# Optimization experiments

Hardware: AMD Instinct MI355X
Metric: run time of the kernel (lower is better)

## Reference

```python
import jax, jax.numpy as jnp
import numpy as np

NQ = 8          # qubits -> 2^8 = 256 amplitudes
B = 32768       # batch

# ---- gate matrices (torchquantum conventions) ----

def _rx(t):
    c = jnp.cos(t / 2).astype(jnp.complex64)
    s = jnp.sin(t / 2).astype(jnp.complex64)
    return jnp.stack([jnp.stack([c, -1j * s]), jnp.stack([-1j * s, c])])

def _ry(t):
    c = jnp.cos(t / 2).astype(jnp.complex64)
    s = jnp.sin(t / 2).astype(jnp.complex64)
    return jnp.stack([jnp.stack([c, -s]), jnp.stack([s, c])])

def _rz(t):
    tc = t.astype(jnp.complex64)
    z = jnp.zeros((), jnp.complex64)
    return jnp.stack([jnp.stack([jnp.exp(-0.5j * tc), z]),
                      jnp.stack([z, jnp.exp(0.5j * tc)])])

def _u3(p):
    th, ph, lm = p[0], p[1], p[2]
    ct = jnp.cos(th / 2).astype(jnp.complex64)
    st = jnp.sin(th / 2).astype(jnp.complex64)
    eip = jnp.exp(1j * ph.astype(jnp.complex64))
    eil = jnp.exp(1j * lm.astype(jnp.complex64))
    return jnp.stack([jnp.stack([ct, -eil * st]),
                      jnp.stack([eip * st, eip * eil * ct])])

# ---- statevector ops; state shape [B] + [2]*NQ ----

def apply_1q(state, U, w):
    s = jnp.moveaxis(state, 1 + w, -1)
    s = jnp.einsum('ij,b...j->b...i', U, s)
    return jnp.moveaxis(s, -1, 1 + w)

def apply_ctrl(state, U, c, t):
    s = jnp.moveaxis(state, (1 + c, 1 + t), (-2, -1))
    s1 = jnp.einsum('ij,b...j->b...i', U, s[..., 1, :])
    s = jnp.concatenate([s[..., :1, :], s1[..., None, :]], axis=-2)
    return jnp.moveaxis(s, (-2, -1), (1 + c, 1 + t))

def expval_z(state, w):
    p = state.real ** 2 + state.imag ** 2
    axes = tuple(i for i in range(1, NQ + 1) if i != 1 + w)
    pm = jnp.sum(p, axis=axes)  # [B, 2]
    return pm[:, 0] - pm[:, 1]

def encode(x):
    # RY angle encoding: product state, amplitude per qubit = (cos(x/2), sin(x/2))
    a = jnp.stack([jnp.cos(x / 2), jnp.sin(x / 2)], -1).astype(jnp.complex64)  # [B,8,2]
    state = a[:, 0]
    for q in range(1, NQ):
        state = jnp.einsum('b...i,bj->b...ij', state, a[:, q])
    return state  # [B,2,2,...,2]

CR_PAIRS_1 = [(0, 1), (2, 3), (4, 5), (6, 7), (1, 2), (3, 4), (5, 6)]
CR_PAIRS_2 = [(1, 3), (5, 7), (3, 5)]

def branch(state, cr_fn, crp, u3p):
    # crp: [10] angles, u3p: [6,3]
    for i, (c, t) in enumerate(CR_PAIRS_1):
        state = apply_ctrl(state, cr_fn(crp[i]), c, t)
    # intermediate tqm.expval calls do not mutate the state -> omitted
    for i, w in enumerate([1, 3, 5, 7]):
        state = apply_1q(state, _u3(u3p[i]), w)
    for i, (c, t) in enumerate(CR_PAIRS_2):
        state = apply_ctrl(state, cr_fn(crp[7 + i]), c, t)
    state = apply_1q(state, _u3(u3p[4]), 3)
    state = apply_1q(state, _u3(u3p[5]), 7)
    return jnp.stack([expval_z(state, 3), expval_z(state, 7)], axis=1)  # [B,2]


def setup_inputs() -> dict:
    key = jax.random.key(0)
    ks = jax.random.split(key, 12)
    pi = np.float32(np.pi)
    u = lambda k, shape: jax.random.uniform(k, shape, jnp.float32, -pi, pi)
    return {
        'x': u(ks[0], (B, NQ)),
        'crx_params': u(ks[1], (10,)),
        'u3x_params': u(ks[2], (6, 3)),
        'cry_params': u(ks[3], (10,)),
        'u3y_params': u(ks[4], (6, 3)),
        'crz_params': u(ks[5], (10,)),
        'u3z_params': u(ks[6], (6, 3)),
        'w1': jax.random.normal(ks[7], (12, 6), jnp.float32) * 0.3,
        'b1': jnp.zeros((12,), jnp.float32),
        'w2': jax.random.normal(ks[8], (1, 12), jnp.float32) * 0.3,
        'b2': jnp.zeros((1,), jnp.float32),
    }


def reference(x, crx_params, u3x_params, cry_params, u3y_params,
              crz_params, u3z_params, w1, b1, w2, b2):
    state = encode(x)
    fx = branch(state, _rx, crx_params, u3x_params)  # CRX branch (qdev)
    fy = branch(state, _ry, cry_params, u3y_params)  # CRY branch (qdev1)
    fz = branch(state, _rz, crz_params, u3z_params)  # CRZ branch (qdev2)
    feats = jnp.concatenate([fx, fy, fz], axis=1)    # [B,6]
    h = jnp.tanh(feats @ w1.T + b1)
    return jax.nn.sigmoid(h @ w2.T + b2)             # [B,1]
```

## Files before the change

kernel.cpp:

```cpp
#include <hip/hip_runtime.h>
#include <math.h>


typedef float v2f __attribute__((ext_vector_type(2)));

__device__ __forceinline__ v2f mk2(float a, float b) { v2f r; r.x = a; r.y = b; return r; }
__device__ __forceinline__ v2f ld2(const float* __restrict__ p) { return *(const v2f*)p; }

__device__ __forceinline__ v2f pk_mul_s(v2f a, v2f b) { v2f d;
  asm("v_pk_mul_f32 %0, %1, %2 op_sel:[0,0] op_sel_hi:[0,1]" : "=v"(d) : "v"(a), "v"(b)); return d; }
__device__ __forceinline__ v2f pk_fma_irot(v2f a, v2f b, v2f c) { v2f d;
  asm("v_pk_fma_f32 %0, %1, %2, %3 op_sel:[1,1,0] op_sel_hi:[1,0,1] neg_lo:[0,1,0]" : "=v"(d) : "v"(a), "v"(b), "v"(c)); return d; }
__device__ __forceinline__ v2f cmul(v2f a, v2f b) { return pk_fma_irot(a, b, pk_mul_s(a, b)); }
__device__ __forceinline__ v2f pk_mul_swap(v2f a, v2f b) { v2f d;
  asm("v_pk_mul_f32 %0, %1, %2 op_sel:[1,0] op_sel_hi:[0,1]" : "=v"(d) : "v"(a), "v"(b)); return d; }

__device__ __forceinline__ v2f pk_mul_sM(v2f M, v2f b) { v2f d;
  asm("v_pk_mul_f32 %0, %1, %2 op_sel:[0,0] op_sel_hi:[0,1]" : "=v"(d) : "s"(M), "v"(b)); return d; }
__device__ __forceinline__ v2f pk_fma_sloM(v2f M, v2f b, v2f c) { v2f d;
  asm("v_pk_fma_f32 %0, %1, %2, %3 op_sel:[0,0,0] op_sel_hi:[0,1,1]" : "=v"(d) : "s"(M), "v"(b), "v"(c)); return d; }
__device__ __forceinline__ v2f pk_fma_shiM(v2f M, v2f b, v2f c) { v2f d;
  asm("v_pk_fma_f32 %0, %1, %2, %3 op_sel:[1,0,0] op_sel_hi:[1,1,1]" : "=v"(d) : "s"(M), "v"(b), "v"(c)); return d; }
__device__ __forceinline__ v2f pk_fma_shi_negM(v2f M, v2f b, v2f c) { v2f d;
  asm("v_pk_fma_f32 %0, %1, %2, %3 op_sel:[1,0,0] op_sel_hi:[1,1,1] neg_lo:[1,0,0] neg_hi:[1,0,0]" : "=v"(d) : "s"(M), "v"(b), "v"(c)); return d; }
__device__ __forceinline__ v2f pk_fma_rotM(v2f M, v2f b, v2f c) { v2f d;
  asm("v_pk_fma_f32 %0, %1, %2, %3 op_sel:[1,1,0] op_sel_hi:[1,0,1] neg_hi:[0,1,0]" : "=v"(d) : "s"(M), "v"(b), "v"(c)); return d; }
__device__ __forceinline__ v2f pk_fma_irotM(v2f M, v2f b, v2f c) { v2f d;
  asm("v_pk_fma_f32 %0, %1, %2, %3 op_sel:[1,1,0] op_sel_hi:[1,0,1] neg_lo:[0,1,0]" : "=v"(d) : "s"(M), "v"(b), "v"(c)); return d; }

template <int MASK>
__device__ __forceinline__ float swz1(float v) {
  constexpr int pat = (MASK << 10) | 0x1F;
  return __int_as_float(__builtin_amdgcn_ds_swizzle(__float_as_int(v), pat));
}
template <int MASK>
__device__ __forceinline__ v2f swz2(v2f v) {
  v2f r; r.x = swz1<MASK>(v.x); r.y = swz1<MASK>(v.y); return r;
}

template <bool A_REAL>
__device__ __forceinline__ v2f u3row_s(v2f ua, v2f ub, v2f a, v2f b) {
  v2f t = pk_mul_sM(ua, a);
  if constexpr (!A_REAL) t = pk_fma_irotM(ua, a, t);
  t = pk_fma_sloM(ub, b, t);
  return pk_fma_irotM(ub, b, t);
}

template <int SB>
__device__ __forceinline__ void u3_apply(v2f w[32], const float* __restrict__ p) {
  const v2f M0 = ld2(p), M1 = ld2(p + 2), M2 = ld2(p + 4), M3 = ld2(p + 6);
#pragma unroll
  for (int i = 0; i < 32; ++i) {
    if (i & (1 << SB)) continue;
    const int i1 = i | (1 << SB);
    const v2f a = w[i], b = w[i1];
    w[i] = u3row_s<true>(M0, M1, a, b);
    w[i1] = u3row_s<false>(M3, M2, b, a);
  }
}

template <int SB, int CB, bool M00R>
__device__ __forceinline__ void u3_sel(v2f w[32], const float* __restrict__ pM,
                                       const float* __restrict__ pN) {
  const v2f M0 = ld2(pM), M1 = ld2(pM + 2), M2 = ld2(pM + 4), M3 = ld2(pM + 6);
  const v2f N0 = ld2(pN), N1 = ld2(pN + 2), N2 = ld2(pN + 4), N3 = ld2(pN + 6);
#pragma unroll
  for (int i = 0; i < 32; ++i) {
    if (i & (1 << SB)) continue;
    const int i1 = i | (1 << SB);
    const v2f a = w[i], b = w[i1];
    if ((i >> CB) & 1) {
      w[i] = u3row_s<false>(N0, N1, a, b);
      w[i1] = u3row_s<false>(N3, N2, b, a);
    } else {
      w[i] = u3row_s<M00R>(M0, M1, a, b);
      w[i1] = u3row_s<false>(M3, M2, b, a);
    }
  }
}

template <int SB, int LB>
__device__ __forceinline__ void crx_Sc_Lt(v2f w[32], v2f cs) {
#pragma unroll
  for (int i = 0; i < 32; ++i) {
    if (!(i & (1 << SB))) continue;
    const v2f p = swz2<(1 << LB)>(w[i]);
    w[i] = pk_fma_rotM(cs, p, pk_mul_sM(cs, w[i]));
  }
}

template <int SB, int LB>
__device__ __forceinline__ void cr_ry_r(float w[32], v2f cs, int gl) {
  const bool tb = (gl >> LB) & 1;
  const float Ky = tb ? cs.y : -cs.y;
#pragma unroll
  for (int i = 0; i < 32; ++i) {
    if (!(i & (1 << SB))) continue;
    const float p = swz1<(1 << LB)>(w[i]);
    w[i] = __builtin_fmaf(Ky, p, cs.x * w[i]);
  }
}

template <int KIND, int SBc, int SBt>
__device__ __forceinline__ void cr_Sc_St(v2f w[32], v2f cs) {
#pragma unroll
  for (int i = 0; i < 32; ++i) {
    if (!(i & (1 << SBc))) continue;
    if constexpr (KIND == 2) {
      const v2f t = pk_mul_sM(cs, w[i]);
      w[i] = (i & (1 << SBt)) ? pk_fma_irotM(cs, w[i], t)
                              : pk_fma_rotM(cs, w[i], t);
    } else {
      if (i & (1 << SBt)) continue;
      const int i1 = i | (1 << SBt);
      const v2f a = w[i], b = w[i1];
      if constexpr (KIND == 0) {
        w[i] = pk_fma_rotM(cs, b, pk_mul_sM(cs, a));
        w[i1] = pk_fma_rotM(cs, a, pk_mul_sM(cs, b));
      } else {
        w[i] = pk_fma_shi_negM(cs, b, pk_mul_sM(cs, a));
        w[i1] = pk_fma_shiM(cs, a, pk_mul_sM(cs, b));
      }
    }
  }
}

template <int SB>
__device__ __forceinline__ void u3_lift(v2f w[32], const float wr[32],
                                        const float* __restrict__ p) {
  const v2f M0 = ld2(p), M1 = ld2(p + 2), M2 = ld2(p + 4), M3 = ld2(p + 6);
#pragma unroll
  for (int i = 0; i < 32; ++i) {
    if (i & (1 << SB)) continue;
    const int i1 = i | (1 << SB);
    const float a = wr[i], b = wr[i1];
    w[i] = mk2(__builtin_fmaf(a, M0.x, b * M1.x), b * M1.y);
    w[i1] = mk2(__builtin_fmaf(a, M2.x, b * M3.x),
                __builtin_fmaf(a, M2.y, b * M3.y));
  }
}

__device__ __forceinline__ void measure2(v2f w[32], const float* __restrict__ q,
                                         v2f res[2]) {
  const v2f qa = ld2(q);
  const v2f qg = ld2(q + 2);
  float z3[2], z7[2];
#pragma unroll
  for (int e = 0; e < 2; ++e) {
    float z3a = 0.f, z3b = 0.f, z7p = 0.f, z7m = 0.f;
#pragma unroll
    for (int s0 = 0; s0 < 16; s0 += 2) {
      const v2f a = w[e * 16 + s0], b = w[e * 16 + s0 + 1];
      const v2f t1 = a * b, t2 = pk_mul_swap(a, b), t3 = a * a, t4 = b * b;
      const float r = t1.x + t1.y;
      const float m = t2.x - t2.y;
      const float na = t3.x + t3.y;
      const float nb = t4.x + t4.y;
      z3a = __builtin_fmaf(qa.x, na, z3a);
      z3b = __builtin_fmaf(qa.y, nb, z3b);
      z3a = __builtin_fmaf(qg.x, r, z3a);
      z3b = __builtin_fmaf(-qg.y, m, z3b);
      const float nn = na + nb;
      if (s0 & 2) z7m += nn; else z7p += nn;
    }
    z3[e] = z3a + z3b;
    z7[e] = z7p - z7m;
  }
  z3[0] += swz1<1>(z3[0]); z3[1] += swz1<1>(z3[1]); z7[0] += swz1<1>(z7[0]); z7[1] += swz1<1>(z7[1]);
  z3[0] += swz1<2>(z3[0]); z3[1] += swz1<2>(z3[1]); z7[0] += swz1<2>(z7[0]); z7[1] += swz1<2>(z7[1]);
  z3[0] += swz1<4>(z3[0]); z3[1] += swz1<4>(z3[1]); z7[0] += swz1<4>(z7[0]); z7[1] += swz1<4>(z7[1]);
  z3[0] += swz1<8>(z3[0]); z3[1] += swz1<8>(z3[1]); z7[0] += swz1<8>(z7[0]); z7[1] += swz1<8>(z7[1]);
  res[0] = mk2(z3[0], z7[0]);
  res[1] = mk2(z3[1], z7[1]);
}

template <int KIND>
__device__ __forceinline__ void tail_common(v2f w[32], const float* __restrict__ Gb,
                                            v2f res[2]) {
  u3_sel<0, 3, true>(w, Gb + 72, Gb + 80);
  u3_apply<2>(w, Gb + 88);
  u3_sel<1, 2, false>(w, Gb + 96, Gb + 104);
  cr_Sc_St<KIND, 0, 2>(w, ld2(Gb + 56));
  measure2(w, Gb + 112, res);
}

__device__ __forceinline__ void load_sincos(const float* __restrict__ xb,
                                            float sn[8], float cn[8]) {
  const float4 xlo = ((const float4*)xb)[0];
  const float4 xhi = ((const float4*)xb)[1];
  const float xq[8] = {xlo.x, xlo.y, xlo.z, xlo.w, xhi.x, xhi.y, xhi.z, xhi.w};
#pragma unroll
  for (int q = 0; q < 8; ++q) __sincosf(0.5f * xq[q], &sn[q], &cn[q]);
}

__device__ __forceinline__ void run_rx(const float* __restrict__ xb0,
                                       const float* __restrict__ xb1,
                                       const float* __restrict__ Gb, int gl,
                                       v2f res[2]) {
  const bool l0 = gl & 1, l1 = (gl >> 1) & 1, l2 = (gl >> 2) & 1, l3 = (gl >> 3) & 1;
  v2f w[32];
#pragma unroll
  for (int e = 0; e < 2; ++e) {
    float sn[8], cn[8];
    load_sincos(e ? xb1 : xb0, sn, cn);
    v2f pa[4], pb[4];
#pragma unroll
    for (int pr = 0; pr < 4; ++pr) {
      const bool lh = (pr == 0) ? l0 : (pr == 1) ? l1 : (pr == 2) ? l2 : l3;
      const float c = Gb[pr * 8], s = Gb[pr * 8 + 1];
      const float uc = lh ? sn[2 * pr] : cn[2 * pr];
      const float b0 = uc * cn[2 * pr + 1], b1 = uc * sn[2 * pr + 1];
      const float Kx = lh ? c : 1.f;
      const float Kyn = lh ? -s : 0.f;
      pa[pr] = mk2(Kx * b0, Kyn * b1);
      pb[pr] = mk2(Kx * b1, Kyn * b0);
    }
    v2f A[4] = {cmul(pa[0], pa[2]), cmul(pa[0], pb[2]), cmul(pb[0], pa[2]), cmul(pb[0], pb[2])};
    v2f Bv[4] = {cmul(pa[3], pa[1]), cmul(pa[3], pb[1]), cmul(pb[3], pa[1]), cmul(pb[3], pb[1])};
#pragma unroll
    for (int s = 0; s < 16; ++s) w[e * 16 + s] = cmul(A[s >> 2], Bv[s & 3]);
  }
  crx_Sc_Lt<3, 1>(w, ld2(Gb + 32));
  crx_Sc_Lt<0, 2>(w, ld2(Gb + 40));
  crx_Sc_Lt<2, 3>(w, ld2(Gb + 48));
  u3_apply<3>(w, Gb + 64);
  tail_common<0>(w, Gb, res);
}

__device__ __forceinline__ void run_ry(const float* __restrict__ xb0,
                                       const float* __restrict__ xb1,
                                       const float* __restrict__ Gb, int gl,
                                       v2f res[2]) {
  const bool l0 = gl & 1, l1 = (gl >> 1) & 1, l2 = (gl >> 2) & 1, l3 = (gl >> 3) & 1;
  float wr[32];
#pragma unroll
  for (int e = 0; e < 2; ++e) {
    float sn[8], cn[8];
    load_sincos(e ? xb1 : xb0, sn, cn);
    float pa[4], pb[4];
#pragma unroll
    for (int pr = 0; pr < 4; ++pr) {
      const bool lh = (pr == 0) ? l0 : (pr == 1) ? l1 : (pr == 2) ? l2 : l3;
      const float c = Gb[pr * 8], s = Gb[pr * 8 + 1];
      const float uc = lh ? sn[2 * pr] : cn[2 * pr];
      const float b0 = uc * cn[2 * pr + 1], b1 = uc * sn[2 * pr + 1];
      const float Kx = lh ? c : 1.f;
      const float Ky = lh ? s : 0.f;
      pa[pr] = Kx * b0 - Ky * b1;
      pb[pr] = Ky * b0 + Kx * b1;
    }
    const float A[4] = {pa[0] * pa[2], pa[0] * pb[2], pb[0] * pa[2], pb[0] * pb[2]};
    const float Bv[4] = {pa[3] * pa[1], pa[3] * pb[1], pb[3] * pa[1], pb[3] * pb[1]};
#pragma unroll
    for (int s = 0; s < 16; ++s) wr[e * 16 + s] = A[s >> 2] * Bv[s & 3];
  }
  cr_ry_r<3, 1>(wr, ld2(Gb + 32), gl);
  cr_ry_r<0, 2>(wr, ld2(Gb + 40), gl);
  cr_ry_r<2, 3>(wr, ld2(Gb + 48), gl);
  v2f w[32];
  u3_lift<3>(w, wr, Gb + 64);
  tail_common<1>(w, Gb, res);
}

__device__ __forceinline__ void run_rz(const float* __restrict__ xb0,
                                       const float* __restrict__ xb1,
                                       const float* __restrict__ Gb, int gl,
                                       v2f res[2]) {
  const bool l0 = gl & 1, l1 = (gl >> 1) & 1, l2 = (gl >> 2) & 1, l3 = (gl >> 3) & 1;
  const float t0 = Gb[2], h0 = Gb[3];
  const float t1 = Gb[10], h1 = Gb[11];
  const float t2 = Gb[18], h2 = Gb[19];
  const float t3 = Gb[26], h3 = Gb[27];
  const float h4 = Gb[35], h5 = Gb[43], h6 = Gb[51];
  const float kk0 = (l1 ? t1 : 0.f) + (l2 ? h5 : -h5);
  const float kk1 = (l3 ? t3 : 0.f);
  const float kk2 = (l2 ? t2 : 0.f) + (l3 ? h6 : -h6);
  const float kk3 = (l0 ? t0 : 0.f) + (l1 ? h4 : -h4);
  const float aa = -((l0 ? h0 : 0.f) + (l1 ? h1 : 0.f) + (l2 ? h2 : 0.f) + (l3 ? h3 : 0.f));
  float v01[2][4], v23[2][4];
#pragma unroll
  for (int e = 0; e < 2; ++e) {
    float sn[8], cn[8];
    load_sincos(e ? xb1 : xb0, sn, cn);
    const float u0 = l0 ? sn[0] : cn[0];
    const float u2 = l1 ? sn[2] : cn[2];
    const float u4 = l2 ? sn[4] : cn[4];
    const float u6 = l3 ? sn[6] : cn[6];
    const float P = (u0 * u2) * (u4 * u6);
    v01[e][0] = P * (cn[3] * cn[7]); v01[e][1] = P * (sn[3] * cn[7]);
    v01[e][2] = P * (cn[3] * sn[7]); v01[e][3] = P * (sn[3] * sn[7]);
    v23[e][0] = cn[5] * cn[1]; v23[e][1] = sn[5] * cn[1];
    v23[e][2] = cn[5] * sn[1]; v23[e][3] = sn[5] * sn[1];
  }
  v2f w[32];
#pragma unroll
  for (int s = 0; s < 16; ++s) {
    float phv = aa;
    if (s & 1) phv += kk0;
    if (s & 2) phv += kk1;
    if (s & 4) phv += kk2;
    if (s & 8) phv += kk3;
    float sp, cp;
    __sincosf(phv, &sp, &cp);
    const float e0 = v01[0][s & 3] * v23[0][s >> 2];
    const float e1 = v01[1][s & 3] * v23[1][s >> 2];
    w[s] = mk2(e0 * cp, e0 * sp);
    w[16 + s] = mk2(e1 * cp, e1 * sp);
  }
  u3_apply<3>(w, Gb + 64);
  tail_common<2>(w, Gb, res);
}

struct c2 { float r, i; };
__device__ __forceinline__ c2 cmulh(c2 a, c2 b) { return {a.r * b.r - a.i * b.i, a.r * b.i + a.i * b.r}; }
__device__ __forceinline__ c2 cmulc(c2 a, c2 b) { return {a.r * b.r + a.i * b.i, a.i * b.r - a.r * b.i}; }
__device__ __forceinline__ c2 caddh(c2 a, c2 b) { return {a.r + b.r, a.i + b.i}; }
__device__ void mat2mul(const c2 A[4], const c2 B[4], c2 C[4]) {
  C[0] = caddh(cmulh(A[0], B[0]), cmulh(A[1], B[2]));
  C[1] = caddh(cmulh(A[0], B[1]), cmulh(A[1], B[3]));
  C[2] = caddh(cmulh(A[2], B[0]), cmulh(A[3], B[2]));
  C[3] = caddh(cmulh(A[2], B[1]), cmulh(A[3], B[3]));
}
__device__ void u3m(const float* p, c2 M[4]) {
  float st, ct, sp, cp, sl, cl;
  sincosf(0.5f * p[0], &st, &ct);
  sincosf(p[1], &sp, &cp);
  sincosf(p[2], &sl, &cl);
  M[0] = {ct, 0.f};
  M[1] = {-cl * st, -sl * st};
  M[2] = {cp * st, sp * st};
  M[3] = {(cp * cl - sp * sl) * ct, (sp * cl + cp * sl) * ct};
}
__device__ void rmat(int kind, float th, c2 R[4]) {
  float s, c;
  sincosf(0.5f * th, &s, &c);
  if (kind == 0) { R[0] = {c, 0.f}; R[1] = {0.f, -s}; R[2] = {0.f, -s}; R[3] = {c, 0.f}; }
  else if (kind == 1) { R[0] = {c, 0.f}; R[1] = {-s, 0.f}; R[2] = {s, 0.f}; R[3] = {c, 0.f}; }
  else { R[0] = {c, -s}; R[1] = {0.f, 0.f}; R[2] = {0.f, 0.f}; R[3] = {c, s}; }
}
__device__ void storeM(float* dst, const c2 M[4]) {
#pragma unroll
  for (int j = 0; j < 4; ++j) { dst[2 * j] = M[j].r; dst[2 * j + 1] = M[j].i; }
}

__global__ void qcnn_prep(const float* __restrict__ crx, const float* __restrict__ u3x,
                          const float* __restrict__ cry, const float* __restrict__ u3y,
                          const float* __restrict__ crz, const float* __restrict__ u3z,
                          float* __restrict__ G) {
  const int br = threadIdx.x;
  if (br >= 3) return;
  const float* crp = (br == 0) ? crx : (br == 1) ? cry : crz;
  const float* u3p = (br == 0) ? u3x : (br == 1) ? u3y : u3z;
  float* Gb = G + br * 128;

  const int crIdx[8] = {0, 1, 2, 3, 4, 5, 6, 9};
#pragma unroll
  for (int i = 0; i < 8; ++i) {
    const float th = crp[crIdx[i]];
    float s, c;
    sincosf(0.5f * th, &s, &c);
    Gb[i * 8] = c;
    Gb[i * 8 + 1] = s;
    Gb[i * 8 + 2] = th;
    Gb[i * 8 + 3] = 0.5f * th;
  }
  c2 U1v[4], U3v[4], U5v[4], U7a[4], U7b[4], U3f[4], R[4], T[4], T2[4];
  u3m(u3p + 0, U1v);
  u3m(u3p + 3, U3v);
  u3m(u3p + 6, U5v);
  u3m(u3p + 9, U7a);
  u3m(u3p + 12, U3f);
  u3m(u3p + 15, U7b);
  storeM(Gb + 64, U1v);
  storeM(Gb + 72, U3v);
  rmat(br, crp[7], R);
  mat2mul(R, U3v, T);
  storeM(Gb + 80, T);
  storeM(Gb + 88, U5v);
  mat2mul(U7b, U7a, T);
  storeM(Gb + 96, T);
  rmat(br, crp[8], R);
  mat2mul(R, U7a, T);
  mat2mul(U7b, T, T2);
  storeM(Gb + 104, T2);
  const float n00 = U3f[0].r * U3f[0].r + U3f[0].i * U3f[0].i;
  const float n01 = U3f[1].r * U3f[1].r + U3f[1].i * U3f[1].i;
  const float n10 = U3f[2].r * U3f[2].r + U3f[2].i * U3f[2].i;
  const float n11 = U3f[3].r * U3f[3].r + U3f[3].i * U3f[3].i;
  const c2 g01 = cmulc(U3f[0], U3f[1]);
  const c2 g23 = cmulc(U3f[2], U3f[3]);
  Gb[112] = n00 - n10;
  Gb[113] = n01 - n11;
  Gb[114] = 2.f * (g01.r - g23.r);
  Gb[115] = 2.f * (g01.i - g23.i);
}

__global__ __launch_bounds__(256) void qcnn_main(
    const float* __restrict__ x, const float* __restrict__ G,
    const float* __restrict__ w1, const float* __restrict__ b1,
    const float* __restrict__ w2, const float* __restrict__ b2,
    float* __restrict__ out, int B) {
  const int gid = blockIdx.x * blockDim.x + threadIdx.x;
  const int grp = gid >> 4;
  const int gl = threadIdx.x & 15;
  const int b0 = grp * 2;
  if (b0 >= B) return;
  const float* xb0 = x + b0 * 8;
  const float* xb1 = x + (b0 + 1) * 8;

  v2f fx[2], fy[2], fz[2];
  run_rx(xb0, xb1, G, gl, fx);
  run_ry(xb0, xb1, G + 128, gl, fy);
  run_rz(xb0, xb1, G + 256, gl, fz);

  const int j = (gl < 12) ? gl : 0;
  const float* w1r = w1 + j * 6;
  const float w10 = w1r[0], w11 = w1r[1], w12 = w1r[2];
  const float w13 = w1r[3], w14 = w1r[4], w15 = w1r[5];
  const float b1v = b1[j], w2v = w2[j], b2v = b2[0];
  float a0 = b1v + w10 * fx[0].x + w11 * fx[0].y + w12 * fy[0].x +
             w13 * fy[0].y + w14 * fz[0].x + w15 * fz[0].y;
  float a1 = b1v + w10 * fx[1].x + w11 * fx[1].y + w12 * fy[1].x +
             w13 * fy[1].y + w14 * fz[1].x + w15 * fz[1].y;
  const float e0 = __expf(2.f * a0), e1 = __expf(2.f * a1);
  const float th0 = 1.f - 2.f * __builtin_amdgcn_rcpf(e0 + 1.f);
  const float th1 = 1.f - 2.f * __builtin_amdgcn_rcpf(e1 + 1.f);
  float t0 = (gl < 12) ? w2v * th0 : 0.f;
  float t1 = (gl < 12) ? w2v * th1 : 0.f;
  t0 += swz1<1>(t0); t1 += swz1<1>(t1);
  t0 += swz1<2>(t0); t1 += swz1<2>(t1);
  t0 += swz1<4>(t0); t1 += swz1<4>(t1);
  t0 += swz1<8>(t0); t1 += swz1<8>(t1);
  const float r0 = __builtin_amdgcn_rcpf(1.f + __expf(-(t0 + b2v)));
  const float r1 = __builtin_amdgcn_rcpf(1.f + __expf(-(t1 + b2v)));
  if (gl == 0) {
    out[b0] = r0;
    out[b0 + 1] = r1;
  }
}

extern "C" void kernel_launch(void* const* d_in, const int* in_sizes, int n_in,
                              void* d_out, int out_size, void* d_ws,
                              size_t ws_size, hipStream_t stream) {
  const float* x = (const float*)d_in[0];
  const float* crx = (const float*)d_in[1];
  const float* u3x = (const float*)d_in[2];
  const float* cry = (const float*)d_in[3];
  const float* u3y = (const float*)d_in[4];
  const float* crz = (const float*)d_in[5];
  const float* u3z = (const float*)d_in[6];
  const float* w1 = (const float*)d_in[7];
  const float* b1 = (const float*)d_in[8];
  const float* w2 = (const float*)d_in[9];
  const float* b2 = (const float*)d_in[10];
  float* out = (float*)d_out;
  float* G = (float*)d_ws;
  const int B = in_sizes[0] / 8;

  hipLaunchKernelGGL(qcnn_prep, dim3(1), dim3(64), 0, stream, crx, u3x, cry,
                     u3y, crz, u3z, G);
  const int ngroups = (B + 1) / 2;
  const int threads = 256;
  const int blocks = (ngroups * 16 + threads - 1) / threads;
  hipLaunchKernelGGL(qcnn_main, dim3(blocks), dim3(threads), 0, stream, x, G,
                     w1, b1, w2, b2, out, B);
}
```

Measured before the change: 106.7 us.

## Split fused kernel into per-branch kernel plus separate MLP kernel

The single kernel that ran all three quantum branches per thread group is split so each block runs only one branch, with three times as many blocks, and writes features to workspace. A separate small kernel then applies the MLP head. The aim is lower register pressure and higher occupancy, since each thread holds one branch's code path. The cost is an extra launch, a global round trip for the features, and redundant encoding of the input across branches. The old fused path stays as a fallback when the workspace is too small.

```diff
diff --git a/kernel.cpp b/kernel.cpp
--- a/kernel.cpp
+++ b/kernel.cpp
@@ -395,6 +395,57 @@
   Gb[115] = 2.f * (g01.i - g23.i);
 }
 
+__global__ __launch_bounds__(256) void qcnn_branch(
+    const float* __restrict__ x, const float* __restrict__ G,
+    float* __restrict__ feats, int B) {
+  const int br = blockIdx.x % 3;
+  const int lb = blockIdx.x / 3;
+  const int gid = lb * blockDim.x + threadIdx.x;
+  const int grp = gid >> 4;
+  const int gl = threadIdx.x & 15;
+  const int b0 = grp * 2;
+  if (b0 >= B) return;
+  const float* xb0 = x + b0 * 8;
+  const float* xb1 = x + (b0 + 1) * 8;
+
+  v2f res[2];
+  if (br == 0)      run_rx(xb0, xb1, G,       gl, res);
+  else if (br == 1) run_ry(xb0, xb1, G + 128, gl, res);
+  else              run_rz(xb0, xb1, G + 256, gl, res);
+
+  if (gl == 0) {
+    *(v2f*)(feats + b0 * 6 + 2 * br) = res[0];
+    *(v2f*)(feats + (b0 + 1) * 6 + 2 * br) = res[1];
+  }
+}
+
+__global__ __launch_bounds__(256) void qcnn_mlp(
+    const float* __restrict__ feats, const float* __restrict__ w1,
+    const float* __restrict__ b1, const float* __restrict__ w2,
+    const float* __restrict__ b2, float* __restrict__ out, int B) {
+  const int b = blockIdx.x * blockDim.x + threadIdx.x;
+  if (b >= B) return;
+  const float* f = feats + b * 6;
+  const v2f f01 = ld2(f), f23 = ld2(f + 2), f45 = ld2(f + 4);
+  const float b2v = b2[0];
+  float acc = b2v;
+#pragma unroll
+  for (int j = 0; j < 12; ++j) {
+    const float* wr = w1 + j * 6;
+    float a = b1[j];
+    a = __builtin_fmaf(wr[0], f01.x, a);
+    a = __builtin_fmaf(wr[1], f01.y, a);
+    a = __builtin_fmaf(wr[2], f23.x, a);
+    a = __builtin_fmaf(wr[3], f23.y, a);
+    a = __builtin_fmaf(wr[4], f45.x, a);
+    a = __builtin_fmaf(wr[5], f45.y, a);
+    const float e = __expf(2.f * a);
+    const float th = 1.f - 2.f * __builtin_amdgcn_rcpf(e + 1.f);
+    acc = __builtin_fmaf(w2[j], th, acc);
+  }
+  out[b] = __builtin_amdgcn_rcpf(1.f + __expf(-acc));
+}
+
 __global__ __launch_bounds__(256) void qcnn_main(
     const float* __restrict__ x, const float* __restrict__ G,
     const float* __restrict__ w1, const float* __restrict__ b1,
@@ -459,9 +510,22 @@
 
   hipLaunchKernelGGL(qcnn_prep, dim3(1), dim3(64), 0, stream, crx, u3x, cry,
                      u3y, crz, u3z, G);
+
   const int ngroups = (B + 1) / 2;
   const int threads = 256;
-  const int blocks = (ngroups * 16 + threads - 1) / threads;
-  hipLaunchKernelGGL(qcnn_main, dim3(blocks), dim3(threads), 0, stream, x, G,
-                     w1, b1, w2, b2, out, B);
-}
+  const size_t need = (size_t)(384 + (size_t)B * 6) * sizeof(float);
+
+  if (ws_size >= need) {
+    float* feats = G + 384;
+    const int bpb = (ngroups * 16 + threads - 1) / threads;
+    hipLaunchKernelGGL(qcnn_branch, dim3(3 * bpb), dim3(threads), 0, stream, x,
+                       G, feats, B);
+    const int mblocks = (B + threads - 1) / threads;
+    hipLaunchKernelGGL(qcnn_mlp, dim3(mblocks), dim3(threads), 0, stream,
+                       feats, w1, b1, w2, b2, out, B);
+  } else {
+    const int blocks = (ngroups * 16 + threads - 1) / threads;
+    hipLaunchKernelGGL(qcnn_main, dim3(blocks), dim3(threads), 0, stream, x, G,
+                       w1, b1, w2, b2, out, B);
+  }
+}
```

Result: slower. 109.4 us (+2.6%).
